# Performance work log

Hardware: AMD Instinct MI355X
Metric: run time of the kernel (lower is better)

## Reference

```python
import jax, jax.numpy as jnp
import numpy as np

D_MODEL = 1024
D_STATE = 64
CHUNK = 256
BATCH = 4
SEQ_LEN = 4096


def setup_inputs() -> dict:
    key = jax.random.key(0)
    k1, k2, k3, k4, k5 = jax.random.split(key, 5)
    u = jax.random.normal(k1, (BATCH, SEQ_LEN, D_MODEL), jnp.float32)
    delta = jax.random.uniform(k2, (BATCH, SEQ_LEN, D_MODEL), jnp.float32)
    B = jax.random.normal(k3, (BATCH, SEQ_LEN, D_STATE), jnp.float32)
    C = jax.random.normal(k4, (BATCH, SEQ_LEN, D_STATE), jnp.float32)
    # matches nn.init.uniform_(A_log, -3.0, -1.0)
    A_log = jax.random.uniform(k5, (D_STATE, D_MODEL), jnp.float32, minval=-3.0, maxval=-1.0)
    return {"u": u, "delta": delta, "B": B, "C": C, "A_log": A_log}


def reference(u, delta, B, C, A_log):
    # delta is accepted but unused, as in the original forward.
    batch, seq_len, d_model = u.shape
    d_state = A_log.shape[0]
    n_chunks = seq_len // CHUNK  # seq_len chosen divisible by chunk_size
    A = -jnp.exp(A_log)  # (N, D)

    # Split sequence into chunks; hidden state resets at each chunk boundary,
    # so all chunks scan independently (vectorized over the n_chunks axis).
    # time-major layout for lax.scan: (CHUNK, batch, n_chunks, ...)
    uc = jnp.moveaxis(u.reshape(batch, n_chunks, CHUNK, d_model), 2, 0)
    Bc = jnp.moveaxis(B.reshape(batch, n_chunks, CHUNK, d_state), 2, 0)
    Cc = jnp.moveaxis(C.reshape(batch, n_chunks, CHUNK, d_state), 2, 0)

    h0 = jnp.zeros((batch, n_chunks, d_state, d_model), u.dtype)

    def step(h, inp):
        x_t, B_t, C_t = inp  # (b,c,D), (b,c,N), (b,c,N)
        h = A * h + B_t[..., :, None] * x_t[..., None, :]  # (b,c,N,D)
        y = jnp.einsum('bcn,bcnd->bcd', C_t, h)             # (b,c,D)
        return h, y

    _, ys = jax.lax.scan(step, h0, (uc, Bc, Cc))  # (CHUNK, b, n_chunks, D)
    out = jnp.moveaxis(ys, 0, 2).reshape(batch, seq_len, d_model)
    return out
```

## Files before the change

kernel.cpp:

```cpp
#include <hip/hip_runtime.h>

typedef float v4 __attribute__((ext_vector_type(4)));

#define D_MODEL 1024
#define D_STATE 64
#define CHUNK   256
#define TILE_T  64

__global__ __launch_bounds__(256, 1)
void YvParallelScan_kernel(const float* __restrict__ u,
                           const float* __restrict__ B,
                           const float* __restrict__ C,
                           const float* __restrict__ A_log,
                           float* __restrict__ out) {
    __shared__ v4 sB[TILE_T * 16];
    __shared__ v4 sC[TILE_T * 16];
    __shared__ v4 sP[2][4][64];

    const int bc   = blockIdx.x >> 2;
    const int dq   = blockIdx.x & 3;
    const int tid  = threadIdx.x;
    const int ng   = tid >> 6;
    const int lane = tid & 63;
    const int rowbase = bc * CHUNK;

    const v4* Bg = (const v4*)(B + (size_t)rowbase * D_STATE);
    const v4* Cg = (const v4*)(C + (size_t)rowbase * D_STATE);

    const int dbase4 = dq * 64 + lane;

    v4 a4[16], h4[16];
#pragma unroll
    for (int j = 0; j < 16; ++j) {
        const int n = ng * 16 + j;
        v4 al = ((const v4*)A_log)[n * 256 + dbase4];
        v4 na;
        na[0] = -__expf(al[0]); na[1] = -__expf(al[1]);
        na[2] = -__expf(al[2]); na[3] = -__expf(al[3]);
        a4[j] = na;
        v4 z = {0.f, 0.f, 0.f, 0.f};
        h4[j] = z;
    }

    const v4* uptr = (const v4*)(u + (size_t)rowbase * D_MODEL) + dbase4;
    v4*       optr = (v4*)(out + (size_t)rowbase * D_MODEL) + dbase4;

    v4 xa = uptr[0];
    v4 xb = uptr[256];

    for (int ti = 0; ti < CHUNK / TILE_T; ++ti) {
#pragma unroll
        for (int k = 0; k < 4; ++k) {
            sB[k * 256 + tid] = Bg[ti * 1024 + k * 256 + tid];
            sC[k * 256 + tid] = Cg[ti * 1024 + k * 256 + tid];
        }
        __syncthreads();

#pragma unroll 4
        for (int tl = 0; tl < TILE_T; ++tl) {
            const int t  = ti * TILE_T + tl;
            const int tp = (t + 2 < CHUNK) ? (t + 2) : (CHUNK - 1);
            v4 xn = uptr[(size_t)tp * 256];

            const v4 x = xa;
            v4 acc = {0.f, 0.f, 0.f, 0.f};
#pragma unroll
            for (int jj = 0; jj < 4; ++jj) {
                v4 b4 = sB[tl * 16 + ng * 4 + jj];
                v4 c4 = sC[tl * 16 + ng * 4 + jj];
#pragma unroll
                for (int k = 0; k < 4; ++k) {
                    const int j = jj * 4 + k;
                    h4[j] = a4[j] * h4[j] + b4[k] * x;
                    acc  += c4[k] * h4[j];
                }
            }

            const int slot = t & 1;
            const int red  = t & 3;
            if (ng != red) sP[slot][ng][lane] = acc;
            __syncthreads();
            if (ng == red) {
                v4 s = acc;
#pragma unroll
                for (int w = 0; w < 4; ++w)
                    if (w != red) s += sP[slot][w][lane];
                optr[(size_t)t * 256] = s;
            }
            xa = xb; xb = xn;
        }
    }
}

extern "C" void kernel_launch(void* const* d_in, const int* in_sizes, int n_in,
                              void* d_out, int out_size, void* d_ws, size_t ws_size,
                              hipStream_t stream) {
    const float* u     = (const float*)d_in[0];
    const float* B     = (const float*)d_in[2];
    const float* C     = (const float*)d_in[3];
    const float* A_log = (const float*)d_in[4];
    float* out = (float*)d_out;

    YvParallelScan_kernel<<<256, 256, 0, stream>>>(u, B, C, A_log, out);
}
```

Baseline: 266.6 us.

## Repartition scan into single-wavefront blocks with DPP cross-lane state reduction

```diff
diff --git a/kernel.cpp b/kernel.cpp
--- a/kernel.cpp
+++ b/kernel.cpp
@@ -5,35 +5,37 @@
 #define D_MODEL 1024
 #define D_STATE 64
 #define CHUNK   256
-#define TILE_T  64
 
-__global__ __launch_bounds__(256, 1)
+__device__ __forceinline__ float dpp_add(float x, int ctrl) {
+    int xi = __float_as_int(x);
+    int yi;
+    switch (ctrl) {
+    case 0xB1:  yi = __builtin_amdgcn_update_dpp(xi, xi, 0xB1,  0xF, 0xF, false); break;
+    case 0x4E:  yi = __builtin_amdgcn_update_dpp(xi, xi, 0x4E,  0xF, 0xF, false); break;
+    default:    yi = __builtin_amdgcn_update_dpp(xi, xi, 0x128, 0xF, 0xF, false); break;
+    }
+    return x + __int_as_float(yi);
+}
+
+__global__ __launch_bounds__(64, 2)
 void YvParallelScan_kernel(const float* __restrict__ u,
                            const float* __restrict__ B,
                            const float* __restrict__ C,
                            const float* __restrict__ A_log,
                            float* __restrict__ out) {
-    __shared__ v4 sB[TILE_T * 16];
-    __shared__ v4 sC[TILE_T * 16];
-    __shared__ v4 sP[2][4][64];
-
-    const int bc   = blockIdx.x >> 2;
-    const int dq   = blockIdx.x & 3;
-    const int tid  = threadIdx.x;
-    const int ng   = tid >> 6;
-    const int lane = tid & 63;
+    const int bc    = blockIdx.x >> 5;
+    const int dseg  = blockIdx.x & 31;
+    const int lane  = threadIdx.x;
+    const int n_grp = (lane & 3) | ((lane & 8) >> 1);
+    const int d_grp = ((lane & 4) >> 2) | ((lane & 48) >> 3);
+    const int d     = dseg * 32 + d_grp * 4;
     const int rowbase = bc * CHUNK;
 
-    const v4* Bg = (const v4*)(B + (size_t)rowbase * D_STATE);
-    const v4* Cg = (const v4*)(C + (size_t)rowbase * D_STATE);
-
-    const int dbase4 = dq * 64 + lane;
-
-    v4 a4[16], h4[16];
+    v4 a4[8], h4[8];
 #pragma unroll
-    for (int j = 0; j < 16; ++j) {
-        const int n = ng * 16 + j;
-        v4 al = ((const v4*)A_log)[n * 256 + dbase4];
+    for (int j = 0; j < 8; ++j) {
+        const int n = n_grp * 8 + j;
+        v4 al = *(const v4*)(A_log + (size_t)n * D_MODEL + d);
         v4 na;
         na[0] = -__expf(al[0]); na[1] = -__expf(al[1]);
         na[2] = -__expf(al[2]); na[3] = -__expf(al[3]);
@@ -42,53 +44,49 @@
         h4[j] = z;
     }
 
-    const v4* uptr = (const v4*)(u + (size_t)rowbase * D_MODEL) + dbase4;
-    v4*       optr = (v4*)(out + (size_t)rowbase * D_MODEL) + dbase4;
+    const v4* uptr = (const v4*)(u + (size_t)rowbase * D_MODEL + d);
+    const v4* Bp   = (const v4*)(B + (size_t)rowbase * D_STATE + n_grp * 8);
+    const v4* Cp   = (const v4*)(C + (size_t)rowbase * D_STATE + n_grp * 8);
+    v4*       optr = (v4*)(out + (size_t)rowbase * D_MODEL + d);
 
-    v4 xa = uptr[0];
-    v4 xb = uptr[256];
+    v4 xa = uptr[0],   xb = uptr[256];
+    v4 Ba0 = Bp[0],  Ba1 = Bp[1],  Ca0 = Cp[0],  Ca1 = Cp[1];
+    v4 Bb0 = Bp[16], Bb1 = Bp[17], Cb0 = Cp[16], Cb1 = Cp[17];
 
-    for (int ti = 0; ti < CHUNK / TILE_T; ++ti) {
+#pragma unroll 2
+    for (int t = 0; t < CHUNK; ++t) {
+        const int tp = (t + 2 < CHUNK) ? (t + 2) : (CHUNK - 1);
+        v4 xn  = uptr[(size_t)tp * 256];
+        v4 Bn0 = Bp[(size_t)tp * 16],     Bn1 = Bp[(size_t)tp * 16 + 1];
+        v4 Cn0 = Cp[(size_t)tp * 16],     Cn1 = Cp[(size_t)tp * 16 + 1];
+
+        const v4 x = xa;
+        v4 acc0 = {0.f, 0.f, 0.f, 0.f};
+        v4 acc1 = {0.f, 0.f, 0.f, 0.f};
+#pragma unroll
+        for (int j = 0; j < 4; ++j) {
+            h4[j]     = a4[j]     * h4[j]     + Ba0[j] * x;
+            acc0     += Ca0[j] * h4[j];
+            h4[4 + j] = a4[4 + j] * h4[4 + j] + Ba1[j] * x;
+            acc1     += Ca1[j] * h4[4 + j];
+        }
+        v4 acc = acc0 + acc1;
+
 #pragma unroll
         for (int k = 0; k < 4; ++k) {
-            sB[k * 256 + tid] = Bg[ti * 1024 + k * 256 + tid];
-            sC[k * 256 + tid] = Cg[ti * 1024 + k * 256 + tid];
+            float s = acc[k];
+            s = dpp_add(s, 0xB1);
+            s = dpp_add(s, 0x4E);
+            s = dpp_add(s, 0x128);
+            acc[k] = s;
         }
-        __syncthreads();
 
-#pragma unroll 4
-        for (int tl = 0; tl < TILE_T; ++tl) {
-            const int t  = ti * TILE_T + tl;
-            const int tp = (t + 2 < CHUNK) ? (t + 2) : (CHUNK - 1);
-            v4 xn = uptr[(size_t)tp * 256];
+        if (n_grp == 0)
+            optr[(size_t)t * 256] = acc;
 
-            const v4 x = xa;
-            v4 acc = {0.f, 0.f, 0.f, 0.f};
-#pragma unroll
-            for (int jj = 0; jj < 4; ++jj) {
-                v4 b4 = sB[tl * 16 + ng * 4 + jj];
-                v4 c4 = sC[tl * 16 + ng * 4 + jj];
-#pragma unroll
-                for (int k = 0; k < 4; ++k) {
-                    const int j = jj * 4 + k;
-                    h4[j] = a4[j] * h4[j] + b4[k] * x;
-                    acc  += c4[k] * h4[j];
-                }
-            }
-
-            const int slot = t & 1;
-            const int red  = t & 3;
-            if (ng != red) sP[slot][ng][lane] = acc;
-            __syncthreads();
-            if (ng == red) {
-                v4 s = acc;
-#pragma unroll
-                for (int w = 0; w < 4; ++w)
-                    if (w != red) s += sP[slot][w][lane];
-                optr[(size_t)t * 256] = s;
-            }
-            xa = xb; xb = xn;
-        }
+        xa = xb; xb = xn;
+        Ba0 = Bb0; Ba1 = Bb1; Ca0 = Cb0; Ca1 = Cb1;
+        Bb0 = Bn0; Bb1 = Bn1; Cb0 = Cn0; Cb1 = Cn1;
     }
 }
 
@@ -101,5 +99,5 @@
     const float* A_log = (const float*)d_in[4];
     float* out = (float*)d_out;
 
-    YvParallelScan_kernel<<<256, 256, 0, stream>>>(u, B, C, A_log, out);
+    YvParallelScan_kernel<<<2048, 64, 0, stream>>>(u, B, C, A_log, out);
 }
```

Result: slower. 293.6 us (+10.1%).
